# Kernel optimization log

Hardware: AMD Instinct MI355X
Metric: run time of the kernel (lower is better)

Reference implementation:

```python
import jax, jax.numpy as jnp
import numpy as np

EMB, HID, SEQ = 768, 512, 2048
BATCH = 2
EPS = 1e-6
LN_EPS = 1e-5
ROPE_BASE = 10000.0
NEG_BIG = -1e9  # stands in for -inf diagonal mask (identical entmax output, NaN-safe)


def rotate_half(x):
    d = x.shape[-1] // 2
    return jnp.concatenate([-x[..., d:], x[..., :d]], axis=-1)


def rope_tables(L, D, dtype=jnp.float32):
    inv_freq = 1.0 / (ROPE_BASE ** (jnp.arange(0, D, 2, dtype=jnp.float32) / D))
    t = jnp.arange(L, dtype=jnp.float32)
    freqs = jnp.outer(t, inv_freq)            # [L, D/2]
    emb = jnp.concatenate([freqs, freqs], -1)  # [L, D]
    return jnp.cos(emb).astype(dtype), jnp.sin(emb).astype(dtype)


def layernorm(x, gamma, beta):
    mu = jnp.mean(x, axis=-1, keepdims=True)
    var = jnp.mean(jnp.square(x - mu), axis=-1, keepdims=True)
    return (x - mu) * jax.lax.rsqrt(var + LN_EPS) * gamma + beta


def entmax15(z):
    """Exact 1.5-entmax along last axis (Peters & Martins sort algorithm)."""
    z = z / 2.0
    z = z - jnp.max(z, axis=-1, keepdims=True)
    zs = -jnp.sort(-z, axis=-1)                      # descending
    L = z.shape[-1]
    k = jnp.arange(1, L + 1, dtype=z.dtype)
    cum = jnp.cumsum(zs, axis=-1)
    cum2 = jnp.cumsum(zs * zs, axis=-1)
    mean = cum / k
    ss = cum2 - cum * mean                           # k*(E[x^2]-E[x]^2)
    delta = (1.0 - ss) / k
    tau = mean - jnp.sqrt(jnp.maximum(delta, 0.0))
    support = jnp.sum((tau <= zs).astype(jnp.int32), axis=-1)
    tau_star = jnp.take_along_axis(tau, (support - 1)[..., None], axis=-1)
    return jnp.square(jnp.maximum(z - tau_star, 0.0))


def setup_inputs() -> dict:
    key = jax.random.key(0)
    ks = jax.random.split(key, 3)
    x = jax.random.normal(ks[0], (BATCH, SEQ, EMB), dtype=jnp.float32)
    Wq = jax.random.normal(ks[1], (HID, EMB), dtype=jnp.float32) / np.sqrt(EMB)
    Wk = jax.random.normal(ks[2], (HID, EMB), dtype=jnp.float32) / np.sqrt(EMB)
    return {
        "x": x, "Wq": Wq, "Wk": Wk,
        "q_gamma": jnp.ones((HID,), jnp.float32), "q_beta": jnp.zeros((HID,), jnp.float32),
        "k_gamma": jnp.ones((HID,), jnp.float32), "k_beta": jnp.zeros((HID,), jnp.float32),
        "C_weight": jnp.ones((1,), jnp.float32),
        "F_weight": jnp.ones((1,), jnp.float32),
        "S_weight": jnp.ones((1,), jnp.float32),
    }


def reference(x, Wq, Wk, q_gamma, q_beta, k_gamma, k_beta, C_weight, F_weight, S_weight):
    B, L, _ = x.shape
    q = layernorm(x @ Wq.T, q_gamma, q_beta)   # [B,L,D]
    k = layernorm(x @ Wk.T, k_gamma, k_beta)
    cos, sin = rope_tables(L, q.shape[-1], q.dtype)
    q = q * cos + rotate_half(q) * sin
    k = k * cos + rotate_half(k) * sin

    wC = 2.0 * jax.nn.sigmoid(C_weight)
    wF = 2.0 * jax.nn.sigmoid(F_weight)
    wS = 2.0 * jax.nn.sigmoid(S_weight)

    Gkk = jnp.einsum('bld,ble->bde', k, k)     # [B,D,D]
    Gkq = jnp.einsum('bld,ble->bde', k, q)
    Gqq = jnp.einsum('bld,ble->bde', q, q)

    C_raw = jnp.einsum('bid,bde,bje->bij', q, Gkk, q)  # [B,L,L]
    F_raw = jnp.einsum('bid,bde,bje->bij', q, Gkq, k)
    S_raw = jnp.einsum('bid,bde,bje->bij', k, Gqq, k)

    C = C_raw - jnp.mean(C_raw, axis=-1, keepdims=True)
    Fm = F_raw - jnp.mean(F_raw, axis=-1, keepdims=True)
    S = S_raw - jnp.mean(S_raw, axis=-1, keepdims=True)

    pC = jnp.clip(entmax15(wC * C), 0.0, 1.0 - EPS)
    pF = jnp.clip(entmax15(wF * Fm), 0.0, 1.0 - EPS)
    pS = jnp.clip(entmax15(wS * S), 0.0, 1.0 - EPS)

    pC = pC * jax.lax.rsqrt(jnp.sum(pC, axis=-2, keepdims=True) + EPS)
    pS = pS * jax.lax.rsqrt(jnp.sum(pS, axis=-2, keepdims=True) + EPS)

    pC = jnp.maximum((1.0 - 2.0 * EPS) * pC + EPS, EPS)
    pF = jnp.maximum((1.0 - 2.0 * EPS) * pF + EPS, EPS)
    pS = jnp.maximum((1.0 - 2.0 * EPS) * pS + EPS, EPS)

    H = (jnp.log(pC) + jnp.log(pF) + jnp.log(pS)) / 3.0
    diag = jnp.eye(L, dtype=bool)[None]
    H = jnp.where(diag, NEG_BIG, H)
    H = entmax15(H)
    return H, pC, pF, pS
```

## Files before the change

kernel.cpp:

```cpp
#include <hip/hip_runtime.h>
#include <cstddef>
#include <math.h>

#define B_   2
#define L_   2048
#define D_   512
#define E_   768
static const size_t LL   = (size_t)L_ * L_;
static const size_t SLOT = (size_t)B_ * LL;

#define QK_N  ((size_t)B_ * L_ * D_)
#define G1_N  ((size_t)512 * 512)
#define G_N   ((size_t)6 * G1_N)
#define U_N   ((size_t)6 * L_ * D_)
#define X_N   ((size_t)4096 * 768)
#define W_N   ((size_t)512 * 768)

typedef unsigned short u16;
typedef __attribute__((ext_vector_type(8))) _Float16 half8;
typedef __attribute__((ext_vector_type(4))) float f32x4;

__device__ __forceinline__ void split2(float f, u16& h0, u16& h1) {
    _Float16 a = (_Float16)f;
    _Float16 b = (_Float16)((f - (float)a) * 4096.0f);
    h0 = __builtin_bit_cast(u16, a);
    h1 = __builtin_bit_cast(u16, b);
}

typedef const __attribute__((address_space(1))) void gas_void;
typedef __attribute__((address_space(3))) void las_void;

__device__ __forceinline__ void gload16(const u16* g, u16* l) {
    __builtin_amdgcn_global_load_lds((gas_void*)g, (las_void*)l, 16, 0, 0);
}

__device__ __forceinline__ void gemm12864p(const u16* __restrict__ Ap, size_t Aps, int lda,
                                           const u16* __restrict__ Bp, size_t Bps, int ldb,
                                           int K, int m0, int n0, int tid,
                                           double outv[4][2][4]) {
    __shared__ u16 SA[2][128][32], SB[2][64][32];
    f32x4 accH[4][2], accM[4][2];
#pragma unroll
    for (int i = 0; i < 4; ++i)
#pragma unroll
        for (int j = 0; j < 2; ++j) {
            accH[i][j] = (f32x4){0.f, 0.f, 0.f, 0.f};
            accM[i][j] = (f32x4){0.f, 0.f, 0.f, 0.f};
        }
    double accD[4][2][4] = {};
    int lane = tid & 63, w = tid >> 6;
    int wm = (w & 1) << 6, wn = (w >> 1) << 5;
    int fr = lane & 15, ko8 = lane >> 4;

    int rbA0 = (w << 5), rbA1 = (w << 5) + 16;
    int rowA0 = rbA0 + (lane >> 2), rowA1 = rbA1 + (lane >> 2);
    int chA0 = (lane & 3) ^ ((rowA0 >> 1) & 3);
    int chA1 = (lane & 3) ^ ((rowA1 >> 1) & 3);
    int rbB = (w << 4);
    int rowB = rbB + (lane >> 2);
    int chB = (lane & 3) ^ ((rowB >> 1) & 3);

    int nstep = K >> 5;
    for (int s = 0; s < nstep; ++s) {
        int k0 = s << 5;
#pragma unroll
        for (int sp = 0; sp < 2; ++sp) {
            gload16(Ap + (size_t)sp * Aps + (size_t)(m0 + rowA0) * lda + k0 + (chA0 << 3),
                    &SA[sp][rbA0][0]);
            gload16(Ap + (size_t)sp * Aps + (size_t)(m0 + rowA1) * lda + k0 + (chA1 << 3),
                    &SA[sp][rbA1][0]);
            gload16(Bp + (size_t)sp * Bps + (size_t)(n0 + rowB) * ldb + k0 + (chB << 3),
                    &SB[sp][rbB][0]);
        }
        __syncthreads();
        half8 a[4][2], b[2][2];
#pragma unroll
        for (int f = 0; f < 4; ++f) {
            int ra = wm + (f << 4) + fr;
            int ca = (ko8 ^ ((ra >> 1) & 3)) << 3;
#pragma unroll
            for (int sp = 0; sp < 2; ++sp)
                a[f][sp] = *reinterpret_cast<const half8*>(&SA[sp][ra][ca]);
        }
#pragma unroll
        for (int f = 0; f < 2; ++f) {
            int rbn = wn + (f << 4) + fr;
            int cb = (ko8 ^ ((rbn >> 1) & 3)) << 3;
#pragma unroll
            for (int sp = 0; sp < 2; ++sp)
                b[f][sp] = *reinterpret_cast<const half8*>(&SB[sp][rbn][cb]);
        }
#pragma unroll
        for (int fi = 0; fi < 4; ++fi)
#pragma unroll
            for (int fj = 0; fj < 2; ++fj) {
                accH[fi][fj] = __builtin_amdgcn_mfma_f32_16x16x32_f16(a[fi][0], b[fj][0], accH[fi][fj], 0, 0, 0);
                accM[fi][fj] = __builtin_amdgcn_mfma_f32_16x16x32_f16(a[fi][0], b[fj][1], accM[fi][fj], 0, 0, 0);
                accM[fi][fj] = __builtin_amdgcn_mfma_f32_16x16x32_f16(a[fi][1], b[fj][0], accM[fi][fj], 0, 0, 0);
            }
        __syncthreads();
#pragma unroll
        for (int fi = 0; fi < 4; ++fi)
#pragma unroll
            for (int fj = 0; fj < 2; ++fj) {
#pragma unroll
                for (int r = 0; r < 4; ++r) accD[fi][fj][r] += (double)accH[fi][fj][r];
                accH[fi][fj] = (f32x4){0.f, 0.f, 0.f, 0.f};
            }
    }
    const double S1 = 1.0 / 4096.0;
#pragma unroll
    for (int fi = 0; fi < 4; ++fi)
#pragma unroll
        for (int fj = 0; fj < 2; ++fj)
#pragma unroll
            for (int r = 0; r < 4; ++r)
                outv[fi][fj][r] = accD[fi][fj][r] + (double)accM[fi][fj][r] * S1;
}

__device__ __forceinline__ void gemm128cv(const u16* __restrict__ Ap, size_t Aps, int lda,
                                          const u16* __restrict__ Bp, size_t Bps, int ldb,
                                          int K, int m0, int n0, int tid,
                                          float* __restrict__ out, int ldo) {
    __shared__ u16 SA[2][2][128][32], SB[2][2][128][32];
    f32x4 accH[4][4], accM[4][4];
#pragma unroll
    for (int i = 0; i < 4; ++i)
#pragma unroll
        for (int j = 0; j < 4; ++j) {
            accH[i][j] = (f32x4){0.f, 0.f, 0.f, 0.f};
            accM[i][j] = (f32x4){0.f, 0.f, 0.f, 0.f};
        }
    int lane = tid & 63, w = tid >> 6;
    int wm = (w & 1) << 6, wn = (w >> 1) << 6;
    int fr = lane & 15, ko8 = lane >> 4;

    int rb0 = (w << 5), rb1 = rb0 + 16;
    int row0 = rb0 + (lane >> 2), row1 = rb1 + (lane >> 2);
    int ch0 = (lane & 3) ^ ((row0 >> 1) & 3);
    int ch1 = (lane & 3) ^ ((row1 >> 1) & 3);

#define STG128(buf, k0)                                                                   \
    {                                                                                     \
        _Pragma("unroll")                                                                 \
        for (int sp = 0; sp < 2; ++sp) {                                                  \
            gload16(Ap + (size_t)sp * Aps + (size_t)(m0 + row0) * lda + (k0) + (ch0 << 3),\
                    &SA[buf][sp][rb0][0]);                                                \
            gload16(Ap + (size_t)sp * Aps + (size_t)(m0 + row1) * lda + (k0) + (ch1 << 3),\
                    &SA[buf][sp][rb1][0]);                                                \
            gload16(Bp + (size_t)sp * Bps + (size_t)(n0 + row0) * ldb + (k0) + (ch0 << 3),\
                    &SB[buf][sp][rb0][0]);                                                \
            gload16(Bp + (size_t)sp * Bps + (size_t)(n0 + row1) * ldb + (k0) + (ch1 << 3),\
                    &SB[buf][sp][rb1][0]);                                                \
        }                                                                                 \
    }

    STG128(0, 0);
    int nstep = K >> 5;
    for (int s = 0; s < nstep; ++s) {
        int cur = s & 1;
        if (s + 1 < nstep) {
            STG128(cur ^ 1, (s + 1) << 5);
            asm volatile("s_waitcnt vmcnt(8)" ::: "memory");
        } else {
            asm volatile("s_waitcnt vmcnt(0)" ::: "memory");
        }
        __builtin_amdgcn_s_barrier();
        asm volatile("" ::: "memory");
        half8 a[4][2], b[4][2];
#pragma unroll
        for (int f = 0; f < 4; ++f) {
            int ra = wm + (f << 4) + fr;
            int rbn = wn + (f << 4) + fr;
            int ca = (ko8 ^ ((ra >> 1) & 3)) << 3;
            int cb = (ko8 ^ ((rbn >> 1) & 3)) << 3;
#pragma unroll
            for (int sp = 0; sp < 2; ++sp) {
                a[f][sp] = *reinterpret_cast<const half8*>(&SA[cur][sp][ra][ca]);
                b[f][sp] = *reinterpret_cast<const half8*>(&SB[cur][sp][rbn][cb]);
            }
        }
        __builtin_amdgcn_s_setprio(1);
#pragma unroll
        for (int fi = 0; fi < 4; ++fi)
#pragma unroll
            for (int fj = 0; fj < 4; ++fj) {
                accH[fi][fj] = __builtin_amdgcn_mfma_f32_16x16x32_f16(a[fi][0], b[fj][0], accH[fi][fj], 0, 0, 0);
                accM[fi][fj] = __builtin_amdgcn_mfma_f32_16x16x32_f16(a[fi][0], b[fj][1], accM[fi][fj], 0, 0, 0);
                accM[fi][fj] = __builtin_amdgcn_mfma_f32_16x16x32_f16(a[fi][1], b[fj][0], accM[fi][fj], 0, 0, 0);
            }
        __builtin_amdgcn_s_setprio(0);
        asm volatile("s_waitcnt lgkmcnt(0)" ::: "memory");
        __builtin_amdgcn_s_barrier();
    }
#undef STG128
    const double S1 = 1.0 / 4096.0;
    int col = lane & 15, rbase = (lane >> 4) << 2;
#pragma unroll
    for (int fi = 0; fi < 4; ++fi)
#pragma unroll
        for (int fj = 0; fj < 4; ++fj)
#pragma unroll
            for (int r = 0; r < 4; ++r) {
                int mm = m0 + wm + (fi << 4) + rbase + r;
                int nn = n0 + wn + (fj << 4) + col;
                out[(size_t)mm * ldo + nn] =
                    (float)((double)accH[fi][fj][r] + (double)accM[fi][fj][r] * S1);
            }
}

__global__ __launch_bounds__(256) void k_prep(const float* __restrict__ x,
                                              const float* __restrict__ Wq,
                                              const float* __restrict__ Wk,
                                              u16* __restrict__ xP,
                                              u16* __restrict__ WP,
                                              double* __restrict__ tg) {
    int bx = blockIdx.x;
    if (bx < L_) {
        int l = bx, j = threadIdx.x;
        double e = (double)j * (1.0 / 256.0);
        double inv = pow(10000.0, -e);
        double ang = (double)l * inv;
        tg[(size_t)l * 512 + j] = cos(ang);
        tg[(size_t)l * 512 + 256 + j] = sin(ang);
        return;
    }
    size_t gid = (size_t)(bx - L_) * 256 + threadIdx.x;
    const size_t XH = X_N / 2, WH = W_N / 2;
    const float* src; u16* dst; size_t pn, off;
    if (gid < XH)            { src = x  + 2 * gid;              dst = xP;            pn = X_N; off = 2 * gid; }
    else if (gid < XH + WH)  { size_t g = gid - XH;      src = Wq + 2 * g; dst = WP;            pn = W_N; off = 2 * g; }
    else                     { size_t g = gid - XH - WH; src = Wk + 2 * g; dst = WP + 2 * W_N;  pn = W_N; off = 2 * g; }
    float2 v = *reinterpret_cast<const float2*>(src);
    u16 a0, a1, b0, b1;
    split2(v.x, a0, a1);
    split2(v.y, b0, b1);
    *reinterpret_cast<unsigned*>(dst + off)      = (unsigned)a0 | ((unsigned)b0 << 16);
    *reinterpret_cast<unsigned*>(dst + pn + off) = (unsigned)a1 | ((unsigned)b1 << 16);
}

__global__ __launch_bounds__(256, 2) void k_proj(const u16* __restrict__ xP,
                                                 const u16* __restrict__ WP,
                                                 float* __restrict__ qraw,
                                                 float* __restrict__ kraw) {
    int z = blockIdx.z;
    float* out = z ? kraw : qraw;
    const u16* Bp = WP + (size_t)z * 2 * W_N;
    gemm128cv(xP, X_N, E_, Bp, W_N, E_, E_,
              blockIdx.y * 128, blockIdx.x * 128, threadIdx.x, out, D_);
}

__global__ __launch_bounds__(256) void k_lnrope(const float* __restrict__ qraw,
                                                const float* __restrict__ kraw,
                                                const double* __restrict__ tg,
                                                const float* __restrict__ qg, const float* __restrict__ qb,
                                                const float* __restrict__ kg, const float* __restrict__ kb,
                                                u16* __restrict__ qP, u16* __restrict__ kP) {
    int row = blockIdx.x;
    int l = row & (L_ - 1);
    int tid = threadIdx.x;
    int half = tid >> 7, t = tid & 127;
    __shared__ double nrow[2][D_];
    __shared__ double red[8];
    __shared__ double cs_[256], sn_[256];
    {
        int j = tid & 255;
        if (tid < 256) { cs_[j] = tg[(size_t)l * 512 + j]; sn_[j] = tg[(size_t)l * 512 + 256 + j]; }
    }
    const float* rp = (half ? kraw : qraw) + (size_t)row * D_;
    const float* g  = half ? kg : qg;
    const float* bt = half ? kb : qb;
    u16* P = half ? kP : qP;
    float4 v = reinterpret_cast<const float4*>(rp)[t];
    double vv[4] = {(double)v.x, (double)v.y, (double)v.z, (double)v.w};
    double s = vv[0] + vv[1] + vv[2] + vv[3];
    double s2 = vv[0]*vv[0] + vv[1]*vv[1] + vv[2]*vv[2] + vv[3]*vv[3];
    for (int off = 32; off; off >>= 1) { s += __shfl_xor(s, off); s2 += __shfl_xor(s2, off); }
    int wv = tid >> 6;
    if ((tid & 63) == 0) { red[wv * 2] = s; red[wv * 2 + 1] = s2; }
    __syncthreads();
    double mu  = (red[half * 4 + 0] + red[half * 4 + 2]) * (1.0 / D_);
    double var = (red[half * 4 + 1] + red[half * 4 + 3]) * (1.0 / D_) - mu * mu;
    double rs = rsqrt(var + 1e-5);
    int d0 = t * 4;
    double o[4];
#pragma unroll
    for (int c = 0; c < 4; ++c) {
        int d = d0 + c;
        o[c] = (vv[c] - mu) * rs * (double)g[d] + (double)bt[d];
    }
#pragma unroll
    for (int c = 0; c < 4; ++c) nrow[half][d0 + c] = o[c];
    __syncthreads();
    u16 h[2][4];
#pragma unroll
    for (int c = 0; c < 4; ++c) {
        int d = d0 + c;
        double rot = (d < 256) ? -nrow[half][d + 256] : nrow[half][d - 256];
        float ov = (float)(nrow[half][d] * cs_[d & 255] + rot * sn_[d & 255]);
        split2(ov, h[0][c], h[1][c]);
    }
    size_t off = (size_t)row * D_ + d0;
#pragma unroll
    for (int sp = 0; sp < 2; ++sp)
        *reinterpret_cast<ushort4*>(P + sp * QK_N + off) = make_ushort4(h[sp][0], h[sp][1], h[sp][2], h[sp][3]);
}

__global__ __launch_bounds__(256) void k_qkT(const u16* __restrict__ qP,
                                             const u16* __restrict__ kP,
                                             u16* __restrict__ qPT,
                                             u16* __restrict__ kPT) {
    __shared__ u16 T[64][72];
    int z = blockIdx.z;
    int b = z & 1, sp = (z >> 1) & 1, tn = z >> 2;
    const u16* src = (tn ? kP : qP) + (size_t)sp * QK_N + (size_t)b * L_ * D_;
    u16* dst       = (tn ? kPT : qPT) + (size_t)sp * QK_N + (size_t)b * D_ * L_;
    int l0 = blockIdx.x * 64, d0 = blockIdx.y * 64;
    int tid = threadIdx.x;
#pragma unroll
    for (int i = 0; i < 2; ++i) {
        int idx = tid + i * 256;
        int lr = idx >> 3, dc8 = (idx & 7) << 3;
        *reinterpret_cast<uint4*>(&T[lr][dc8]) =
            *reinterpret_cast<const uint4*>(&src[(size_t)(l0 + lr) * D_ + d0 + dc8]);
    }
    __syncthreads();
#pragma unroll
    for (int i = 0; i < 2; ++i) {
        int idx = tid + i * 256;
        int dr = idx >> 3, lc8 = (idx & 7) << 3;
        u16 tmp[8];
#pragma unroll
        for (int c = 0; c < 8; ++c) tmp[c] = T[lc8 + c][dr];
        *reinterpret_cast<uint4*>(&dst[(size_t)(d0 + dr) * L_ + l0 + lc8]) =
            *reinterpret_cast<const uint4*>(tmp);
    }
}

__global__ __launch_bounds__(256, 2) void k_gram(const u16* __restrict__ qPT,
                                                 const u16* __restrict__ kPT,
                                                 float* __restrict__ Gpart) {
    int zz = blockIdx.z, half = zz & 1, z = zz >> 1;
    int b = z / 3, m = z % 3;
    const u16* A  = ((m == 2) ? qPT : kPT) + (size_t)b * D_ * L_ + (size_t)half * (L_ / 2);
    const u16* Bp = ((m == 0) ? kPT : qPT) + (size_t)b * D_ * L_ + (size_t)half * (L_ / 2);
    int m0 = blockIdx.y * 128, n0 = blockIdx.x * 64;
    double ov[4][2][4];
    gemm12864p(A, QK_N, L_, Bp, QK_N, L_, L_ / 2, m0, n0, threadIdx.x, ov);
    float* Gg = Gpart + (size_t)half * G_N + (size_t)z * G1_N;
    int lane = threadIdx.x & 63, w = threadIdx.x >> 6;
    int wm = (w & 1) << 6, wn = (w >> 1) << 5;
    int col = lane & 15, rbase = (lane >> 4) << 2;
#pragma unroll
    for (int fi = 0; fi < 4; ++fi)
#pragma unroll
        for (int fj = 0; fj < 2; ++fj)
#pragma unroll
            for (int r = 0; r < 4; ++r) {
                int mm = m0 + wm + fi * 16 + rbase + r;
                int nn = n0 + wn + fj * 16 + col;
                Gg[(size_t)mm * 512 + nn] = (float)ov[fi][fj][r];
            }
}

__global__ __launch_bounds__(256) void k_gsplitT(const float* __restrict__ Gpart,
                                                 u16* __restrict__ GPT) {
    __shared__ float T[64][65];
    int z = blockIdx.z, d0 = blockIdx.y * 64, e0 = blockIdx.x * 64;
    const float* Ga = Gpart + (size_t)z * G1_N;
    const float* Gb = Ga + G_N;
    int tid = threadIdx.x;
#pragma unroll
    for (int i = 0; i < 16; ++i) {
        int idx = tid + i * 256;
        int r = idx >> 6, c = idx & 63;
        size_t o = (size_t)(d0 + r) * 512 + e0 + c;
        T[r][c] = Ga[o] + Gb[o];
    }
    __syncthreads();
    u16* Gz = GPT + (size_t)z * G1_N;
#pragma unroll
    for (int i = 0; i < 16; ++i) {
        int idx = tid + i * 256;
        int er = idx >> 6, dc = idx & 63;
        u16 h0, h1; split2(T[dc][er], h0, h1);
        size_t o = (size_t)(e0 + er) * 512 + d0 + dc;
        Gz[o] = h0; Gz[G_N + o] = h1;
    }
}

__global__ __launch_bounds__(256, 2) void k_u(const u16* __restrict__ qP,
                                              const u16* __restrict__ kP,
                                              const u16* __restrict__ GPT,
                                              u16* __restrict__ UP) {
    int z = blockIdx.z, b = z / 3, m = z % 3;
    const u16* A  = ((m == 2) ? kP : qP) + (size_t)b * L_ * D_;
    const u16* Bp = GPT + (size_t)z * G1_N;
    int m0 = blockIdx.y * 128, n0 = blockIdx.x * 64;
    double ov[4][2][4];
    gemm12864p(A, QK_N, D_, Bp, G_N, 512, D_, m0, n0, threadIdx.x, ov);
    int lane = threadIdx.x & 63, w = threadIdx.x >> 6;
    int wm = (w & 1) << 6, wn = (w >> 1) << 5;
    int col = lane & 15, rbase = (lane >> 4) << 2;
#pragma unroll
    for (int fi = 0; fi < 4; ++fi)
#pragma unroll
        for (int fj = 0; fj < 2; ++fj)
#pragma unroll
            for (int r = 0; r < 4; ++r) {
                float uf = (float)ov[fi][fj][r];
                int mm = m0 + wm + fi * 16 + rbase + r;
                int nn = n0 + wn + fj * 16 + col;
                size_t off = (size_t)z * ((size_t)L_ * D_) + (size_t)mm * D_ + nn;
                u16 h0, h1; split2(uf, h0, h1);
                UP[off] = h0; UP[U_N + off] = h1;
            }
}

__global__ __launch_bounds__(256, 2) void k_scores(const u16* __restrict__ qP,
                                                   const u16* __restrict__ kP,
                                                   const u16* __restrict__ UP,
                                                   float* __restrict__ out) {
    int z = blockIdx.z, b = z / 3, m = z % 3;
    const u16* A  = UP + (size_t)z * ((size_t)L_ * D_);
    const u16* Bp = ((m == 0) ? qP : kP) + (size_t)b * L_ * D_;
    float* Co = out + (size_t)(1 + m) * SLOT + (size_t)b * LL;
    gemm128cv(A, U_N, D_, Bp, QK_N, D_, D_,
              blockIdx.y * 128, blockIdx.x * 128, threadIdx.x, Co, L_);
}

__global__ __launch_bounds__(256) void k_entmax(float* __restrict__ base, int nrows,
                                                const float* __restrict__ wC,
                                                const float* __restrict__ wF,
                                                const float* __restrict__ wS) {
    int tid = threadIdx.x;
    int lane = tid & 63;
    int r = blockIdx.x * 4 + (tid >> 6);
    if (r >= nrows) return;
    int m = r >> 12;
    const float* wp = (m == 0) ? wC : (m == 1) ? wF : wS;
    float hw = (float)(1.0 / (1.0 + exp(-(double)wp[0])));
    float* row = base + (size_t)r * L_;
    float v[32];
    float mx = -3.4e38f;
#pragma unroll
    for (int j = 0; j < 32; ++j) {
        v[j] = row[lane + (j << 6)];
        mx = fmaxf(mx, v[j]);
    }
    for (int off = 32; off; off >>= 1) mx = fmaxf(mx, __shfl_xor(mx, off));
    float z[32];
#pragma unroll
    for (int j = 0; j < 32; ++j) z[j] = hw * (v[j] - mx);
    float lo = -1.0f, hi = 0.0f;
    for (int it = 0; it < 9; ++it) {
        float tau = 0.5f * (lo + hi);
        float ssum = 0.0f;
#pragma unroll
        for (int j = 0; j < 32; ++j) {
            float t = fmaxf(z[j] - tau, 0.0f);
            ssum = fmaf(t, t, ssum);
        }
        for (int off = 32; off; off >>= 1) ssum += __shfl_xor(ssum, off);
        if (ssum >= 1.0f) lo = tau; else hi = tau;
    }
    float tau = lo;
    for (int it = 0; it < 3; ++it) {
        float s1 = 0.0f, s2 = 0.0f;
#pragma unroll
        for (int j = 0; j < 32; ++j) {
            float t = fmaxf(z[j] - tau, 0.0f);
            s1 += t;
            s2 = fmaf(t, t, s2);
        }
        for (int off = 32; off; off >>= 1) { s1 += __shfl_xor(s1, off); s2 += __shfl_xor(s2, off); }
        float denom = 2.0f * s1;
        if (denom > 1e-30f) tau += fmaxf((s2 - 1.0f) / denom, 0.0f);
    }
#pragma unroll
    for (int j = 0; j < 32; ++j) {
        float t = fmaxf(z[j] - tau, 0.0f);
        row[lane + (j << 6)] = fminf(t * t, 1.0f - 1e-6f);
    }
}

__global__ __launch_bounds__(256) void k_colsum(const float* __restrict__ out,
                                                double* __restrict__ part) {
    int bz = blockIdx.z, which = bz >> 1, b = bz & 1;
    const float* mat = out + (size_t)(which ? 3 : 1) * SLOT + (size_t)b * LL;
    int j = blockIdx.x * 256 + threadIdx.x;
    int r0 = blockIdx.y * 128;
    double s = 0.0;
#pragma unroll 8
    for (int r = 0; r < 128; ++r) s += (double)mat[(size_t)(r0 + r) * L_ + j];
    part[((size_t)bz * 16 + blockIdx.y) * L_ + j] = s;
}

__global__ __launch_bounds__(256) void k_colred(const double* __restrict__ part,
                                                double* __restrict__ csC,
                                                double* __restrict__ csS) {
    int g = blockIdx.x * 256 + threadIdx.x;
    int bz = g >> 11, j = g & (L_ - 1);
    int which = bz >> 1, b = bz & 1;
    double s = 0.0;
#pragma unroll
    for (int c = 0; c < 16; ++c) s += part[((size_t)bz * 16 + c) * L_ + j];
    (which ? csS : csC)[b * L_ + j] = s;
}

__global__ __launch_bounds__(256) void k_fin2(float* __restrict__ out,
                                              const double* __restrict__ csC,
                                              const double* __restrict__ csS) {
    int row = blockIdx.x;
    int i = row & (L_ - 1), b = row >> 11;
    size_t ro = (size_t)row * L_;
    float* H  = out + ro;
    float* pC = out + SLOT + ro;
    float* pF = out + 2 * SLOT + ro;
    float* pS = out + 3 * SLOT + ro;
    const double* cc = csC + b * L_;
    const double* cs = csS + b * L_;
    int tid = threadIdx.x, lane = tid & 63, wv = tid >> 6;
    __shared__ float red[4], red2[4];
    const double A1 = 1.0 - 2e-6;
    float h[8];
    float mx = -3.4e38f;
#pragma unroll
    for (int c = 0; c < 8; ++c) {
        int j = (c << 8) + tid;
        double cv = (double)pC[j] * rsqrt(cc[j] + 1e-6);
        double fv = (double)pF[j];
        double sv = (double)pS[j] * rsqrt(cs[j] + 1e-6);
        cv = fmax(A1 * cv + 1e-6, 1e-6);
        fv = fmax(A1 * fv + 1e-6, 1e-6);
        sv = fmax(A1 * sv + 1e-6, 1e-6);
        pC[j] = (float)cv; pF[j] = (float)fv; pS[j] = (float)sv;
        h[c] = (j == i) ? -1e9f : logf((float)(cv * fv * sv)) * (1.0f / 3.0f);
        mx = fmaxf(mx, h[c]);
    }
    for (int off = 32; off; off >>= 1) mx = fmaxf(mx, __shfl_xor(mx, off));
    if (lane == 0) red[wv] = mx;
    __syncthreads();
    mx = fmaxf(fmaxf(red[0], red[1]), fmaxf(red[2], red[3]));
    __syncthreads();
    float z[8];
#pragma unroll
    for (int c = 0; c < 8; ++c) z[c] = 0.5f * (h[c] - mx);
    float lo = -1.0f, hi = 0.0f;
    for (int it = 0; it < 9; ++it) {
        float tau = 0.5f * (lo + hi);
        float ssum = 0.0f;
#pragma unroll
        for (int c = 0; c < 8; ++c) {
            float t = fmaxf(z[c] - tau, 0.0f);
            ssum = fmaf(t, t, ssum);
        }
        for (int off = 32; off; off >>= 1) ssum += __shfl_xor(ssum, off);
        if (lane == 0) red[wv] = ssum;
        __syncthreads();
        ssum = red[0] + red[1] + red[2] + red[3];
        __syncthreads();
        if (ssum >= 1.0f) lo = tau; else hi = tau;
    }
    float tau = lo;
    for (int it = 0; it < 3; ++it) {
        float s1 = 0.0f, s2 = 0.0f;
#pragma unroll
        for (int c = 0; c < 8; ++c) {
            float t = fmaxf(z[c] - tau, 0.0f);
            s1 += t;
            s2 = fmaf(t, t, s2);
        }
        for (int off = 32; off; off >>= 1) { s1 += __shfl_xor(s1, off); s2 += __shfl_xor(s2, off); }
        if (lane == 0) { red[wv] = s1; red2[wv] = s2; }
        __syncthreads();
        s1 = red[0] + red[1] + red[2] + red[3];
        s2 = red2[0] + red2[1] + red2[2] + red2[3];
        __syncthreads();
        float denom = 2.0f * s1;
        if (denom > 1e-30f) tau += fmaxf((s2 - 1.0f) / denom, 0.0f);
    }
#pragma unroll
    for (int c = 0; c < 8; ++c) {
        float t = fmaxf(z[c] - tau, 0.0f);
        H[(c << 8) + tid] = t * t;
    }
}

extern "C" void kernel_launch(void* const* d_in, const int* in_sizes, int n_in,
                              void* d_out, int out_size, void* d_ws, size_t ws_size,
                              hipStream_t stream) {
    const float* x  = (const float*)d_in[0];
    const float* Wq = (const float*)d_in[1];
    const float* Wk = (const float*)d_in[2];
    const float* qg = (const float*)d_in[3];
    const float* qb = (const float*)d_in[4];
    const float* kg = (const float*)d_in[5];
    const float* kb = (const float*)d_in[6];
    const float* wC = (const float*)d_in[7];
    const float* wF = (const float*)d_in[8];
    const float* wS = (const float*)d_in[9];
    float* out = (float*)d_out;

    char* wsb = (char*)d_ws;
    u16*    UP   = (u16*)wsb;
    float*  qraw = (float*)wsb;
    float*  kraw = qraw + QK_N;
    u16*    qPT  = (u16*)wsb;
    u16*    kPT  = qPT + 2 * QK_N;
    float*  Gpart = (float*)(wsb + 2 * QK_N * sizeof(float));
    wsb += 3 * U_N * sizeof(u16);
    u16*    qP    = (u16*)wsb;
    u16*    xP    = (u16*)wsb;   wsb += 3 * QK_N * sizeof(u16);
    u16*    kP    = (u16*)wsb;   wsb += 3 * QK_N * sizeof(u16);
    u16*    GPT   = (u16*)wsb;
    u16*    WP    = (u16*)wsb;   wsb += 3 * G_N * sizeof(u16);
    double* tg    = (double*)wsb;
    double* part  = tg;
    double* csC   = tg + (size_t)4 * 16 * L_;
    double* csS   = csC + (size_t)B_ * L_;

    k_prep    <<<dim3(L_ + 7680), 256, 0, stream>>>(x, Wq, Wk, xP, WP, tg);
    k_proj    <<<dim3(4, 32, 2),  256, 0, stream>>>(xP, WP, qraw, kraw);
    k_lnrope  <<<dim3(B_ * L_),   256, 0, stream>>>(qraw, kraw, tg, qg, qb, kg, kb, qP, kP);
    k_qkT     <<<dim3(32, 8, 8),  256, 0, stream>>>(qP, kP, qPT, kPT);
    k_gram    <<<dim3(8, 4, 12),  256, 0, stream>>>(qPT, kPT, Gpart);
    k_gsplitT <<<dim3(8, 8, 6),   256, 0, stream>>>(Gpart, GPT);
    k_u       <<<dim3(8, 16, 6),  256, 0, stream>>>(qP, kP, GPT, UP);
    k_scores  <<<dim3(16, 16, 6), 256, 0, stream>>>(qP, kP, UP, out);
    k_entmax  <<<dim3(3072),      256, 0, stream>>>(out + SLOT, 3 * B_ * L_, wC, wF, wS);
    k_colsum  <<<dim3(8, 16, 4),  256, 0, stream>>>(out, part);
    k_colred  <<<dim3(32),        256, 0, stream>>>(part, csC, csS);
    k_fin2    <<<dim3(B_ * L_),   256, 0, stream>>>(out, csC, csS);
}
```

Measured before the change: 472.9 us.

## Exploit symmetry of C and S score matrices, compute upper triangle and mirror

C_raw and S_raw are symmetric (q Gkk q^T and k Gqq k^T), so the scores kernel now computes only the lower-triangular 128x128 tiles for those two and writes each off-diagonal tile twice, the second time transposed through shared memory. The grid becomes a flat 1D launch with a triangular index decode. This cuts the GEMM work for two of the three score matrices by nearly half. In exchange it adds extra barriers and transposed stores per mirrored tile, and the result relies on the symmetry holding closely enough numerically.

Result: faster. 450.5 us (median of 2 runs) (-4.7%).

```diff
diff --git a/kernel.cpp b/kernel.cpp
--- a/kernel.cpp
+++ b/kernel.cpp
@@ -121,8 +121,11 @@
 __device__ __forceinline__ void gemm128cv(const u16* __restrict__ Ap, size_t Aps, int lda,
                                           const u16* __restrict__ Bp, size_t Bps, int ldb,
                                           int K, int m0, int n0, int tid,
-                                          float* __restrict__ out, int ldo) {
-    __shared__ u16 SA[2][2][128][32], SB[2][2][128][32];
+                                          float* __restrict__ out, int ldo,
+                                          bool mirror) {
+    __shared__ u16 SRAW[32768];
+#define IDXA(buf, sp, row) (((((buf) * 2 + (sp)) * 128) + (row)) * 32)
+#define IDXB(buf, sp, row) (16384 + ((((buf) * 2 + (sp)) * 128) + (row)) * 32)
     f32x4 accH[4][4], accM[4][4];
 #pragma unroll
     for (int i = 0; i < 4; ++i)
@@ -145,13 +148,13 @@
         _Pragma("unroll")                                                                 \
         for (int sp = 0; sp < 2; ++sp) {                                                  \
             gload16(Ap + (size_t)sp * Aps + (size_t)(m0 + row0) * lda + (k0) + (ch0 << 3),\
-                    &SA[buf][sp][rb0][0]);                                                \
+                    &SRAW[IDXA(buf, sp, rb0)]);                                           \
             gload16(Ap + (size_t)sp * Aps + (size_t)(m0 + row1) * lda + (k0) + (ch1 << 3),\
-                    &SA[buf][sp][rb1][0]);                                                \
+                    &SRAW[IDXA(buf, sp, rb1)]);                                           \
             gload16(Bp + (size_t)sp * Bps + (size_t)(n0 + row0) * ldb + (k0) + (ch0 << 3),\
-                    &SB[buf][sp][rb0][0]);                                                \
+                    &SRAW[IDXB(buf, sp, rb0)]);                                           \
             gload16(Bp + (size_t)sp * Bps + (size_t)(n0 + row1) * ldb + (k0) + (ch1 << 3),\
-                    &SB[buf][sp][rb1][0]);                                                \
+                    &SRAW[IDXB(buf, sp, rb1)]);                                           \
         }                                                                                 \
     }
 
@@ -176,8 +179,8 @@
             int cb = (ko8 ^ ((rbn >> 1) & 3)) << 3;
 #pragma unroll
             for (int sp = 0; sp < 2; ++sp) {
-                a[f][sp] = *reinterpret_cast<const half8*>(&SA[cur][sp][ra][ca]);
-                b[f][sp] = *reinterpret_cast<const half8*>(&SB[cur][sp][rbn][cb]);
+                a[f][sp] = *reinterpret_cast<const half8*>(&SRAW[IDXA(cur, sp, ra) + ca]);
+                b[f][sp] = *reinterpret_cast<const half8*>(&SRAW[IDXB(cur, sp, rbn) + cb]);
             }
         }
         __builtin_amdgcn_s_setprio(1);
@@ -207,6 +210,34 @@
                 out[(size_t)mm * ldo + nn] =
                     (float)((double)accH[fi][fj][r] + (double)accM[fi][fj][r] * S1);
             }
+    if (mirror) {
+        float* TF = (float*)SRAW;
+        int hsel = wm >> 6;
+#pragma unroll
+        for (int h = 0; h < 2; ++h) {
+            __syncthreads();
+            if (hsel == h) {
+#pragma unroll
+                for (int fi = 0; fi < 4; ++fi)
+#pragma unroll
+                    for (int fj = 0; fj < 4; ++fj)
+#pragma unroll
+                        for (int r = 0; r < 4; ++r) {
+                            float v = (float)((double)accH[fi][fj][r] + (double)accM[fi][fj][r] * S1);
+                            TF[((fi << 4) + rbase + r) * 129 + wn + (fj << 4) + col] = v;
+                        }
+            }
+            __syncthreads();
+#pragma unroll
+            for (int i = 0; i < 32; ++i) {
+                int idx = (i << 8) + tid;
+                int tr = idx >> 6, tc = idx & 63;
+                out[(size_t)(n0 + tr) * ldo + m0 + (h << 6) + tc] = TF[tc * 129 + tr];
+            }
+        }
+    }
+#undef IDXA
+#undef IDXB
 }
 
 __global__ __launch_bounds__(256) void k_prep(const float* __restrict__ x,
@@ -247,7 +278,7 @@
     float* out = z ? kraw : qraw;
     const u16* Bp = WP + (size_t)z * 2 * W_N;
     gemm128cv(xP, X_N, E_, Bp, W_N, E_, E_,
-              blockIdx.y * 128, blockIdx.x * 128, threadIdx.x, out, D_);
+              blockIdx.y * 128, blockIdx.x * 128, threadIdx.x, out, D_, false);
 }
 
 __global__ __launch_bounds__(256) void k_lnrope(const float* __restrict__ qraw,
@@ -421,12 +452,29 @@
                                                    const u16* __restrict__ kP,
                                                    const u16* __restrict__ UP,
                                                    float* __restrict__ out) {
-    int z = blockIdx.z, b = z / 3, m = z % 3;
+    int bid = blockIdx.x;
+    int b = bid / 528, r = bid % 528;
+    int m, I, J;
+    if (r < 136) {
+        m = 0;
+        int t = r, i = 0;
+        while ((i + 1) * (i + 2) / 2 <= t) ++i;
+        I = i; J = t - i * (i + 1) / 2;
+    } else if (r < 392) {
+        m = 1; I = (r - 136) >> 4; J = (r - 136) & 15;
+    } else {
+        m = 2;
+        int t = r - 392, i = 0;
+        while ((i + 1) * (i + 2) / 2 <= t) ++i;
+        I = i; J = t - i * (i + 1) / 2;
+    }
+    int z = b * 3 + m;
     const u16* A  = UP + (size_t)z * ((size_t)L_ * D_);
     const u16* Bp = ((m == 0) ? qP : kP) + (size_t)b * L_ * D_;
     float* Co = out + (size_t)(1 + m) * SLOT + (size_t)b * LL;
+    bool mir = (m != 1) && (I != J);
     gemm128cv(A, U_N, D_, Bp, QK_N, D_, D_,
-              blockIdx.y * 128, blockIdx.x * 128, threadIdx.x, Co, L_);
+              I * 128, J * 128, threadIdx.x, Co, L_, mir);
 }
 
 __global__ __launch_bounds__(256) void k_entmax(float* __restrict__ base, int nrows,
@@ -627,7 +675,7 @@
     k_gram    <<<dim3(8, 4, 12),  256, 0, stream>>>(qPT, kPT, Gpart);
     k_gsplitT <<<dim3(8, 8, 6),   256, 0, stream>>>(Gpart, GPT);
     k_u       <<<dim3(8, 16, 6),  256, 0, stream>>>(qP, kP, GPT, UP);
-    k_scores  <<<dim3(16, 16, 6), 256, 0, stream>>>(qP, kP, UP, out);
+    k_scores  <<<dim3(1056),      256, 0, stream>>>(qP, kP, UP, out);
     k_entmax  <<<dim3(3072),      256, 0, stream>>>(out + SLOT, 3 * B_ * L_, wC, wF, wS);
     k_colsum  <<<dim3(8, 16, 4),  256, 0, stream>>>(out, part);
     k_colred  <<<dim3(32),        256, 0, stream>>>(part, csC, csS);
```
